# Optimization experiments

Measured on AMD Instinct MI355X. Metric: run time of the kernel, lower is better.

Reference implementation:

```python
import jax, jax.numpy as jnp
import numpy as np

B, D_W, D_C, D_P = 4096, 2048, 1024, 2048
RANK = D_W // 4  # 512, per A_U/A_V shapes (d_w, d_w//4)


def setup_inputs() -> dict:
    key = jax.random.key(0)
    ks = jax.random.split(key, 10)
    return {
        "w_prev": jax.random.normal(ks[0], (B, D_W), jnp.float32),
        "z_t": jax.random.normal(ks[1], (B, D_P), jnp.float32),
        "c_t": jax.random.normal(ks[2], (B, D_C), jnp.float32),
        # params (mirroring flax init: A_diag zeros, A_U/A_V normal(0.01),
        # Dense kernels lecun_normal-ish scale, zero biases)
        "A_diag": jnp.zeros((D_W,), jnp.float32),
        "A_U": 0.01 * jax.random.normal(ks[3], (D_W, RANK), jnp.float32),
        "A_V": 0.01 * jax.random.normal(ks[4], (D_W, RANK), jnp.float32),
        "W_mod": jax.random.normal(ks[5], (D_C, D_W), jnp.float32) / np.sqrt(D_C),
        "b_mod": jnp.zeros((D_W,), jnp.float32),
        "W_B": jax.random.normal(ks[6], (D_C + D_P, D_W), jnp.float32) / np.sqrt(D_C + D_P),
        "b_B": jnp.zeros((D_W,), jnp.float32),
    }


def reference(w_prev, z_t, c_t, A_diag, A_U, A_V, W_mod, b_mod, W_B, b_B):
    # A = diag(tanh(A_diag)*0.9) + A_U @ A_V^T, row-scaled by modulation.
    # Equivalent (same math) without materializing [B, d_w, d_w]:
    #   (A * m[:, :, None]) @ w = m * (a_diag * w + A_U @ (A_V^T @ w))
    a_diag = jnp.tanh(A_diag) * 0.9                              # [d_w]
    modulation = jnp.tanh(c_t @ W_mod + b_mod)                   # [B, d_w]
    Aw = a_diag * w_prev + (w_prev @ A_V) @ A_U.T                # [B, d_w]
    Bt = jnp.concatenate([c_t, z_t], axis=-1) @ W_B + b_B        # [B, d_w]
    return modulation * Aw + Bt
```

## Files before the change

### kernel.cpp

```cpp
#include <hip/hip_runtime.h>


#define DEV __device__ __forceinline__

typedef __bf16 v8bf __attribute__((ext_vector_type(8)));
typedef __bf16 v4bf __attribute__((ext_vector_type(4)));
typedef float  v4f  __attribute__((ext_vector_type(4)));

typedef __attribute__((address_space(1))) const unsigned int* as1_cuint_ptr;
typedef __attribute__((address_space(3))) unsigned int*       as3_uint_ptr;

DEV void async16(const void* g, void* l) {
  __builtin_amdgcn_global_load_lds(
      (as1_cuint_ptr)(unsigned long long)g,
      (as3_uint_ptr)(unsigned long long)l,
      16, 0, 0);
}

DEV float tanh_fast(float x) {
  x = fminf(15.f, fmaxf(-15.f, x));
  float e = __expf(2.f * x);
  return (e - 1.f) / (e + 1.f);
}

__global__ __launch_bounds__(256, 2) void prep_gemm(
    const float* __restrict__ w, const float* __restrict__ z,
    const float* __restrict__ c, const float* __restrict__ au,
    const float* __restrict__ av, const float* __restrict__ Wmod,
    const float* __restrict__ WB, const float* __restrict__ A_diag,
    __bf16* __restrict__ wb, __bf16* __restrict__ zb, __bf16* __restrict__ cb,
    __bf16* __restrict__ Wmodt, __bf16* __restrict__ WBt,
    __bf16* __restrict__ Mt) {
  __shared__ __align__(16) char smem[16384];
  int b = blockIdx.x;

  if (b < 256) {
    __bf16* As = (__bf16*)smem;
    __bf16* Bs = (__bf16*)(smem + 8192);
    const int tid = threadIdx.x, lane = tid & 63, wid = tid >> 6;
    const int wm = wid >> 1, wn = wid & 1, l16 = lane & 15, quad = lane >> 4;
    const int m0 = (b >> 4) * 128, n0 = (b & 15) * 128;
    const int qs = quad ^ ((l16 >> 1) & 3);
    const int row = tid >> 1, sp = (tid & 1) * 2;

    v4f acc[4][4];
#pragma unroll
    for (int i = 0; i < 4; ++i)
#pragma unroll
      for (int j = 0; j < 4; ++j) { v4f zz = {0, 0, 0, 0}; acc[i][j] = zz; }

    for (int k0 = 0; k0 < 512; k0 += 32) {
      __syncthreads();
#pragma unroll
      for (int ss = 0; ss < 2; ++ss) {
        const int s = sp + ss;
        const int gk = (s ^ ((row >> 1) & 3)) * 8;
        const float* pa = au + (size_t)(m0 + row) * 512 + k0 + gk;
        const float* pb = av + (size_t)(n0 + row) * 512 + k0 + gk;
        float4 a0 = *reinterpret_cast<const float4*>(pa);
        float4 a1 = *reinterpret_cast<const float4*>(pa + 4);
        float4 b0 = *reinterpret_cast<const float4*>(pb);
        float4 b1 = *reinterpret_cast<const float4*>(pb + 4);
        v8bf va, vb;
        va[0] = (__bf16)a0.x; va[1] = (__bf16)a0.y;
        va[2] = (__bf16)a0.z; va[3] = (__bf16)a0.w;
        va[4] = (__bf16)a1.x; va[5] = (__bf16)a1.y;
        va[6] = (__bf16)a1.z; va[7] = (__bf16)a1.w;
        vb[0] = (__bf16)b0.x; vb[1] = (__bf16)b0.y;
        vb[2] = (__bf16)b0.z; vb[3] = (__bf16)b0.w;
        vb[4] = (__bf16)b1.x; vb[5] = (__bf16)b1.y;
        vb[6] = (__bf16)b1.z; vb[7] = (__bf16)b1.w;
        *reinterpret_cast<v8bf*>(&As[row * 32 + s * 8]) = va;
        *reinterpret_cast<v8bf*>(&Bs[row * 32 + s * 8]) = vb;
      }
      __syncthreads();
      const v8bf* Ap = reinterpret_cast<const v8bf*>(As);
      const v8bf* Bp = reinterpret_cast<const v8bf*>(Bs);
      v8bf a[4], bb[4];
#pragma unroll
      for (int i = 0; i < 4; ++i) a[i] = Ap[(wm * 64 + i * 16 + l16) * 4 + qs];
#pragma unroll
      for (int j = 0; j < 4; ++j) bb[j] = Bp[(wn * 64 + j * 16 + l16) * 4 + qs];
#pragma unroll
      for (int i = 0; i < 4; ++i)
#pragma unroll
        for (int j = 0; j < 4; ++j)
          acc[i][j] = __builtin_amdgcn_mfma_f32_16x16x32_bf16(a[i], bb[j],
                                                              acc[i][j], 0, 0, 0);
    }

    const int mBase = m0 + wm * 64 + quad * 4;
    const int nBase = n0 + wn * 64 + l16;
#pragma unroll
    for (int j = 0; j < 4; ++j) {
      const int n = nBase + j * 16;
#pragma unroll
      for (int i = 0; i < 4; ++i)
#pragma unroll
        for (int r = 0; r < 4; ++r) {
          const int m = mBase + i * 16 + r;
          float v = acc[i][j][r];
          if (m == n) v += tanh_fast(A_diag[m]) * 0.9f;
          Mt[(size_t)m * 2048 + n] = (__bf16)v;
        }
    }
    return;
  }

  b -= 256;
  if (b < 20480) {
    const float* src; __bf16* dst; int off;
    if (b < 8192)       { src = w; dst = wb; off = b; }
    else if (b < 16384) { src = z; dst = zb; off = b - 8192; }
    else                { src = c; dst = cb; off = b - 16384; }
    size_t i = (size_t)off * 1024 + (size_t)threadIdx.x * 4;
    float4 v = *reinterpret_cast<const float4*>(src + i);
    v4bf o;
    o.x = (__bf16)v.x; o.y = (__bf16)v.y; o.z = (__bf16)v.z; o.w = (__bf16)v.w;
    *reinterpret_cast<v4bf*>(dst + i) = o;
    return;
  }

  b -= 20480;
  float (*t)[33] = (float(*)[33])smem;
  const float* src; __bf16* dst; int R;
  if (b < 2048) { src = Wmod; dst = Wmodt; R = 1024; }
  else          { b -= 2048; src = WB; dst = WBt; R = 3072; }
  const int c0 = (b & 63) * 32, r0 = (b >> 6) * 32;
  const int C = 2048;
  const int tx = threadIdx.x & 31, ty = threadIdx.x >> 5;
#pragma unroll
  for (int rr = 0; rr < 32; rr += 8)
    t[ty + rr][tx] = src[(size_t)(r0 + ty + rr) * C + c0 + tx];
  __syncthreads();
  const int orow = threadIdx.x >> 3;
  const int oc   = (threadIdx.x & 7) * 4;
  v4bf o;
  o.x = (__bf16)t[oc + 0][orow];
  o.y = (__bf16)t[oc + 1][orow];
  o.z = (__bf16)t[oc + 2][orow];
  o.w = (__bf16)t[oc + 3][orow];
  *reinterpret_cast<v4bf*>(&dst[(size_t)(c0 + orow) * R + r0 + oc]) = o;
}

__global__ __launch_bounds__(256, 2) void fused_main(
    const __bf16* __restrict__ c, const __bf16* __restrict__ z,
    const __bf16* __restrict__ w, const __bf16* __restrict__ Wmodt,
    const __bf16* __restrict__ Mt, const __bf16* __restrict__ WBt,
    const float* __restrict__ b_mod, const float* __restrict__ b_B,
    float* __restrict__ out) {
  constexpr int DC = 1024, DW = 2048, KB = 3072;
  __shared__ __align__(16) __bf16 As[128 * 128];
  __shared__ __align__(16) __bf16 Bs[128 * 128];

  const int tid = threadIdx.x, lane = tid & 63, wid = tid >> 6;
  const int wm = wid >> 1, wn = wid & 1, l16 = lane & 15, quad = lane >> 4;
  const int m0 = blockIdx.y * 128;
  const int n0 = blockIdx.x * 128;
  const int r4  = lane >> 4;
  const int s16 = lane & 15;

  v4f acc[4][4];
#pragma unroll
  for (int i = 0; i < 4; ++i)
#pragma unroll
    for (int j = 0; j < 4; ++j) { v4f zz = {0,0,0,0}; acc[i][j] = zz; }

  auto kstep = [&](const __bf16* gA, size_t lda, const __bf16* gB, size_t ldb,
                   int kA, int kB) {
    __syncthreads();
#pragma unroll
    for (int t = 0; t < 8; ++t) {
      const int row = wid * 32 + t * 4 + r4;
      const int gk = (s16 ^ (row & 15)) * 8;
      async16((const void*)(gA + (size_t)(m0 + row) * lda + kA + gk),
              (void*)&As[row * 128 + s16 * 8]);
      async16((const void*)(gB + (size_t)(n0 + row) * ldb + kB + gk),
              (void*)&Bs[row * 128 + s16 * 8]);
    }
    __syncthreads();
    const v8bf* Ap = reinterpret_cast<const v8bf*>(As);
    const v8bf* Bp = reinterpret_cast<const v8bf*>(Bs);
#pragma unroll
    for (int s = 0; s < 4; ++s) {
      const int rs = (s * 4 + quad) ^ l16;
      v8bf a[4], b[4];
#pragma unroll
      for (int i = 0; i < 4; ++i)
        a[i] = Ap[(wm * 64 + i * 16 + l16) * 16 + rs];
#pragma unroll
      for (int j = 0; j < 4; ++j)
        b[j] = Bp[(wn * 64 + j * 16 + l16) * 16 + rs];
#pragma unroll
      for (int i = 0; i < 4; ++i)
#pragma unroll
        for (int j = 0; j < 4; ++j)
          acc[i][j] = __builtin_amdgcn_mfma_f32_16x16x32_bf16(
              a[i], b[j], acc[i][j], 0, 0, 0);
    }
  };

  const int nBase = n0 + wn * 64 + l16;

  for (int k0 = 0; k0 < DC; k0 += 128) kstep(c, DC, Wmodt, DC, k0, k0);

  v4f mod_s[4][4];
#pragma unroll
  for (int j = 0; j < 4; ++j) {
    const float bn = b_mod[nBase + j * 16];
#pragma unroll
    for (int i = 0; i < 4; ++i) {
#pragma unroll
      for (int r = 0; r < 4; ++r)
        mod_s[i][j][r] = tanh_fast(acc[i][j][r] + bn);
      v4f zz = {0,0,0,0};
      acc[i][j] = zz;
    }
  }

  for (int k0 = 0; k0 < DW; k0 += 128) kstep(w, DW, Mt, DW, k0, k0);

#pragma unroll
  for (int i = 0; i < 4; ++i)
#pragma unroll
    for (int j = 0; j < 4; ++j) acc[i][j] *= mod_s[i][j];

  for (int k0 = 0; k0 < DC; k0 += 128) kstep(c, DC, WBt, KB, k0, k0);
  for (int k0 = DC; k0 < KB; k0 += 128) kstep(z, DW, WBt, KB, k0 - DC, k0);

  const int mBase = m0 + wm * 64 + quad * 4;
#pragma unroll
  for (int j = 0; j < 4; ++j) {
    const int n = nBase + j * 16;
    const float bn = b_B[n];
#pragma unroll
    for (int i = 0; i < 4; ++i)
#pragma unroll
      for (int r = 0; r < 4; ++r) {
        const int m = mBase + i * 16 + r;
        out[(size_t)m * DW + n] = acc[i][j][r] + bn;
      }
  }
}


extern "C" void kernel_launch(void* const* d_in, const int* in_sizes, int n_in,
                              void* d_out, int out_size, void* d_ws,
                              size_t ws_size, hipStream_t stream) {
  const float* w_prev = (const float*)d_in[0];
  const float* z_t    = (const float*)d_in[1];
  const float* c_t    = (const float*)d_in[2];
  const float* A_diag = (const float*)d_in[3];
  const float* A_U    = (const float*)d_in[4];
  const float* A_V    = (const float*)d_in[5];
  const float* W_mod  = (const float*)d_in[6];
  const float* b_mod  = (const float*)d_in[7];
  const float* W_B    = (const float*)d_in[8];
  const float* b_B    = (const float*)d_in[9];

  constexpr int Bsz = 4096, DW = 2048;
  const size_t MB = 1ull << 20;
  char* ws = (char*)d_ws;
  __bf16* w_bf  = (__bf16*)(ws + 0);
  __bf16* z_bf  = (__bf16*)(ws + 16 * MB);
  __bf16* c_bf  = (__bf16*)(ws + 32 * MB);
  __bf16* Wmodt = (__bf16*)(ws + 40 * MB);
  __bf16* WBt   = (__bf16*)(ws + 44 * MB);
  __bf16* Mt    = (__bf16*)(ws + 56 * MB);

  prep_gemm<<<28928, 256, 0, stream>>>(w_prev, z_t, c_t, A_U, A_V, W_mod, W_B,
                                       A_diag, w_bf, z_bf, c_bf, Wmodt, WBt,
                                       Mt);

  fused_main<<<dim3(DW / 128, Bsz / 128), 256, 0, stream>>>(
      c_bf, z_bf, w_bf, Wmodt, Mt, WBt, b_mod, b_B, (float*)d_out);
}
```

Measured before the change: 285.3 us.

## Pipeline main GEMM with triple-buffered async loads and 256x128 tiles

Rewrites the fused GEMM kernel to use 512-thread blocks with 256x128 output tiles, a 64-wide K step and a three-stage LDS ring, so async global-to-LDS loads for tile t+2 overlap the MFMA work on tile t. It also swizzles block order for L2 locality, keeps the modulation factor in bf16 registers, and makes the prep kernel grid-stride over fewer blocks. The aim is to hide the load-wait-compute serialization and per-step barriers of the old single-buffer loop. In exchange it needs more LDS and registers per block and uses hand-placed vmcnt waits and barriers, which could cost occupancy or break if the wait counts are wrong.

```diff
diff --git a/kernel.cpp b/kernel.cpp
--- a/kernel.cpp
+++ b/kernel.cpp
@@ -108,138 +108,206 @@
   }
 
   b -= 256;
-  if (b < 20480) {
-    const float* src; __bf16* dst; int off;
-    if (b < 8192)       { src = w; dst = wb; off = b; }
-    else if (b < 16384) { src = z; dst = zb; off = b - 8192; }
-    else                { src = c; dst = cb; off = b - 16384; }
-    size_t i = (size_t)off * 1024 + (size_t)threadIdx.x * 4;
-    float4 v = *reinterpret_cast<const float4*>(src + i);
-    v4bf o;
-    o.x = (__bf16)v.x; o.y = (__bf16)v.y; o.z = (__bf16)v.z; o.w = (__bf16)v.w;
-    *reinterpret_cast<v4bf*>(dst + i) = o;
+  if (b < 2048) {
+    for (int u = b; u < 20480; u += 2048) {
+      const float* src; __bf16* dst; int off;
+      if (u < 8192)       { src = w; dst = wb; off = u; }
+      else if (u < 16384) { src = z; dst = zb; off = u - 8192; }
+      else                { src = c; dst = cb; off = u - 16384; }
+      size_t i = (size_t)off * 1024 + (size_t)threadIdx.x * 4;
+      float4 v = *reinterpret_cast<const float4*>(src + i);
+      v4bf o;
+      o.x = (__bf16)v.x; o.y = (__bf16)v.y;
+      o.z = (__bf16)v.z; o.w = (__bf16)v.w;
+      *reinterpret_cast<v4bf*>(dst + i) = o;
+    }
     return;
   }
 
-  b -= 20480;
+  b -= 2048;
   float (*t)[33] = (float(*)[33])smem;
-  const float* src; __bf16* dst; int R;
-  if (b < 2048) { src = Wmod; dst = Wmodt; R = 1024; }
-  else          { b -= 2048; src = WB; dst = WBt; R = 3072; }
-  const int c0 = (b & 63) * 32, r0 = (b >> 6) * 32;
-  const int C = 2048;
   const int tx = threadIdx.x & 31, ty = threadIdx.x >> 5;
-#pragma unroll
-  for (int rr = 0; rr < 32; rr += 8)
-    t[ty + rr][tx] = src[(size_t)(r0 + ty + rr) * C + c0 + tx];
-  __syncthreads();
   const int orow = threadIdx.x >> 3;
   const int oc   = (threadIdx.x & 7) * 4;
-  v4bf o;
-  o.x = (__bf16)t[oc + 0][orow];
-  o.y = (__bf16)t[oc + 1][orow];
-  o.z = (__bf16)t[oc + 2][orow];
-  o.w = (__bf16)t[oc + 3][orow];
-  *reinterpret_cast<v4bf*>(&dst[(size_t)(c0 + orow) * R + r0 + oc]) = o;
-}
-
-__global__ __launch_bounds__(256, 2) void fused_main(
+  for (int u = b; u < 8192; u += 1024) {
+    const float* src; __bf16* dst; int R, uu = u;
+    if (uu < 2048) { src = Wmod; dst = Wmodt; R = 1024; }
+    else           { uu -= 2048; src = WB; dst = WBt; R = 3072; }
+    const int c0 = (uu & 63) * 32, r0 = (uu >> 6) * 32;
+    const int C = 2048;
+    __syncthreads();
+#pragma unroll
+    for (int rr = 0; rr < 32; rr += 8)
+      t[ty + rr][tx] = src[(size_t)(r0 + ty + rr) * C + c0 + tx];
+    __syncthreads();
+    v4bf o;
+    o.x = (__bf16)t[oc + 0][orow];
+    o.y = (__bf16)t[oc + 1][orow];
+    o.z = (__bf16)t[oc + 2][orow];
+    o.w = (__bf16)t[oc + 3][orow];
+    *reinterpret_cast<v4bf*>(&dst[(size_t)(c0 + orow) * R + r0 + oc]) = o;
+  }
+}
+
+__global__ __launch_bounds__(512, 2) void fused_main(
     const __bf16* __restrict__ c, const __bf16* __restrict__ z,
     const __bf16* __restrict__ w, const __bf16* __restrict__ Wmodt,
     const __bf16* __restrict__ Mt, const __bf16* __restrict__ WBt,
     const float* __restrict__ b_mod, const float* __restrict__ b_B,
     float* __restrict__ out) {
-  constexpr int DC = 1024, DW = 2048, KB = 3072;
-  __shared__ __align__(16) __bf16 As[128 * 128];
-  __shared__ __align__(16) __bf16 Bs[128 * 128];
+  constexpr int DC = 1024, DW = 2048, KB3 = 3072;
+  constexpr int ATE = 256 * 64;
+  constexpr int BTE = 128 * 64;
+  constexpr int NT = 96;
+  __shared__ __align__(16) __bf16 As[3 * ATE];
+  __shared__ __align__(16) __bf16 Bs[3 * BTE];
 
   const int tid = threadIdx.x, lane = tid & 63, wid = tid >> 6;
-  const int wm = wid >> 1, wn = wid & 1, l16 = lane & 15, quad = lane >> 4;
-  const int m0 = blockIdx.y * 128;
-  const int n0 = blockIdx.x * 128;
-  const int r4  = lane >> 4;
-  const int s16 = lane & 15;
+  const int wm = wid >> 1, wn = wid & 1;
+  const int l16 = lane & 15, quad = lane >> 4, l8 = l16 & 7;
+  const int s8 = tid & 7, rowi = tid >> 3;
+  const int gks = ((s8 ^ (rowi & 7)) << 3);
+
+  const int flat = blockIdx.y * 16 + blockIdx.x;
+  const int swz = (flat & 7) * 32 + (flat >> 3);
+  const int m0 = (swz >> 4) * 256;
+  const int n0 = (swz & 15) * 128;
+
+  const int nBase = n0 + wn * 64 + l16;
+  float bmodr[4], bBr[4];
+#pragma unroll
+  for (int j = 0; j < 4; ++j) {
+    bmodr[j] = b_mod[nBase + j * 16];
+    bBr[j]   = b_B[nBase + j * 16];
+  }
+
+  auto resolve = [&](int T, const __bf16*& gA, int& lda, int& kA,
+                     const __bf16*& gB, int& ldb, int& kB) {
+    if (T < 16)      { gA = c; lda = DC; kA = T << 6;        gB = Wmodt; ldb = DC;  kB = T << 6; }
+    else if (T < 48) { gA = w; lda = DW; kA = (T - 16) << 6; gB = Mt;    ldb = DW;  kB = (T - 16) << 6; }
+    else if (T < 64) { gA = c; lda = DC; kA = (T - 48) << 6; gB = WBt;   ldb = KB3; kB = (T - 48) << 6; }
+    else             { gA = z; lda = DW; kA = (T - 64) << 6; gB = WBt;   ldb = KB3; kB = DC + ((T - 64) << 6); }
+  };
+
+  auto stageA = [&](int T, int q0, int qn) {
+    const __bf16* gA; const __bf16* gB; int lda, ldb, kA, kB;
+    resolve(T, gA, lda, kA, gB, ldb, kB);
+    __bf16* Ab = &As[(T % 3) * ATE];
+#pragma unroll
+    for (int q = 0; q < 4; ++q) {
+      if (q < q0 || q >= q0 + qn) continue;
+      const int row = q * 64 + rowi;
+      async16((const void*)(gA + (size_t)(m0 + row) * lda + kA + gks),
+              (void*)&Ab[row * 64 + s8 * 8]);
+    }
+  };
+  auto stageB = [&](int T) {
+    const __bf16* gA; const __bf16* gB; int lda, ldb, kA, kB;
+    resolve(T, gA, lda, kA, gB, ldb, kB);
+    __bf16* Bb = &Bs[(T % 3) * BTE];
+#pragma unroll
+    for (int q = 0; q < 2; ++q) {
+      const int row = q * 64 + rowi;
+      async16((const void*)(gB + (size_t)(n0 + row) * ldb + kB + gks),
+              (void*)&Bb[row * 64 + s8 * 8]);
+    }
+  };
 
   v4f acc[4][4];
 #pragma unroll
   for (int i = 0; i < 4; ++i)
 #pragma unroll
-    for (int j = 0; j < 4; ++j) { v4f zz = {0,0,0,0}; acc[i][j] = zz; }
-
-  auto kstep = [&](const __bf16* gA, size_t lda, const __bf16* gB, size_t ldb,
-                   int kA, int kB) {
-    __syncthreads();
-#pragma unroll
-    for (int t = 0; t < 8; ++t) {
-      const int row = wid * 32 + t * 4 + r4;
-      const int gk = (s16 ^ (row & 15)) * 8;
-      async16((const void*)(gA + (size_t)(m0 + row) * lda + kA + gk),
-              (void*)&As[row * 128 + s16 * 8]);
-      async16((const void*)(gB + (size_t)(n0 + row) * ldb + kB + gk),
-              (void*)&Bs[row * 128 + s16 * 8]);
-    }
-    __syncthreads();
-    const v8bf* Ap = reinterpret_cast<const v8bf*>(As);
-    const v8bf* Bp = reinterpret_cast<const v8bf*>(Bs);
-#pragma unroll
-    for (int s = 0; s < 4; ++s) {
-      const int rs = (s * 4 + quad) ^ l16;
-      v8bf a[4], b[4];
+    for (int j = 0; j < 4; ++j) { v4f zz = {0, 0, 0, 0}; acc[i][j] = zz; }
+  v4bf mod_b[4][4];
+
+  stageA(0, 0, 4); stageB(0);
+  stageA(1, 0, 4); stageB(1);
+  asm volatile("s_waitcnt vmcnt(6)" ::: "memory");
+  __builtin_amdgcn_s_barrier();
+  asm volatile("" ::: "memory");
+
+  for (int t = 0; t < NT; ++t) {
+    const v8bf* Ap = reinterpret_cast<const v8bf*>(&As[(t % 3) * ATE]);
+    const v8bf* Bp = reinterpret_cast<const v8bf*>(&Bs[(t % 3) * BTE]);
+    const bool pre = (t + 2 < NT);
+
+    v8bf a0[4], b0[4];
+#pragma unroll
+    for (int i = 0; i < 4; ++i)
+      a0[i] = Ap[(wm * 64 + i * 16 + l16) * 8 + (quad ^ l8)];
+#pragma unroll
+    for (int j = 0; j < 4; ++j)
+      b0[j] = Bp[(wn * 64 + j * 16 + l16) * 8 + (quad ^ l8)];
+    if (pre) stageA(t + 2, 0, 3);
+    asm volatile("" ::: "memory");
+    __builtin_amdgcn_s_barrier();
+    __builtin_amdgcn_s_setprio(1);
+#pragma unroll
+    for (int i = 0; i < 4; ++i)
+#pragma unroll
+      for (int j = 0; j < 4; ++j)
+        acc[i][j] = __builtin_amdgcn_mfma_f32_16x16x32_bf16(a0[i], b0[j],
+                                                            acc[i][j], 0, 0, 0);
+    __builtin_amdgcn_s_setprio(0);
+    asm volatile("" ::: "memory");
+    __builtin_amdgcn_s_barrier();
+
+    v8bf a1[4], b1[4];
+#pragma unroll
+    for (int i = 0; i < 4; ++i)
+      a1[i] = Ap[(wm * 64 + i * 16 + l16) * 8 + ((4 + quad) ^ l8)];
+#pragma unroll
+    for (int j = 0; j < 4; ++j)
+      b1[j] = Bp[(wn * 64 + j * 16 + l16) * 8 + ((4 + quad) ^ l8)];
+    if (pre) { stageA(t + 2, 3, 1); stageB(t + 2); }
+    asm volatile("" ::: "memory");
+    __builtin_amdgcn_s_barrier();
+    __builtin_amdgcn_s_setprio(1);
+#pragma unroll
+    for (int i = 0; i < 4; ++i)
+#pragma unroll
+      for (int j = 0; j < 4; ++j)
+        acc[i][j] = __builtin_amdgcn_mfma_f32_16x16x32_bf16(a1[i], b1[j],
+                                                            acc[i][j], 0, 0, 0);
+    __builtin_amdgcn_s_setprio(0);
+    if (pre) asm volatile("s_waitcnt vmcnt(6)" ::: "memory");
+    else     asm volatile("s_waitcnt vmcnt(0)" ::: "memory");
+    __builtin_amdgcn_s_barrier();
+    asm volatile("" ::: "memory");
+
+    if (t == 15) {
 #pragma unroll
       for (int i = 0; i < 4; ++i)
-        a[i] = Ap[(wm * 64 + i * 16 + l16) * 16 + rs];
-#pragma unroll
-      for (int j = 0; j < 4; ++j)
-        b[j] = Bp[(wn * 64 + j * 16 + l16) * 16 + rs];
+#pragma unroll
+        for (int j = 0; j < 4; ++j) {
+          v4bf mb;
+#pragma unroll
+          for (int r = 0; r < 4; ++r)
+            mb[r] = (__bf16)tanh_fast(acc[i][j][r] + bmodr[j]);
+          mod_b[i][j] = mb;
+          v4f zz = {0, 0, 0, 0};
+          acc[i][j] = zz;
+        }
+    } else if (t == 47) {
 #pragma unroll
       for (int i = 0; i < 4; ++i)
 #pragma unroll
         for (int j = 0; j < 4; ++j)
-          acc[i][j] = __builtin_amdgcn_mfma_f32_16x16x32_bf16(
-              a[i], b[j], acc[i][j], 0, 0, 0);
-    }
-  };
-
-  const int nBase = n0 + wn * 64 + l16;
-
-  for (int k0 = 0; k0 < DC; k0 += 128) kstep(c, DC, Wmodt, DC, k0, k0);
-
-  v4f mod_s[4][4];
-#pragma unroll
-  for (int j = 0; j < 4; ++j) {
-    const float bn = b_mod[nBase + j * 16];
-#pragma unroll
-    for (int i = 0; i < 4; ++i) {
-#pragma unroll
-      for (int r = 0; r < 4; ++r)
-        mod_s[i][j][r] = tanh_fast(acc[i][j][r] + bn);
-      v4f zz = {0,0,0,0};
-      acc[i][j] = zz;
-    }
-  }
-
-  for (int k0 = 0; k0 < DW; k0 += 128) kstep(w, DW, Mt, DW, k0, k0);
-
-#pragma unroll
-  for (int i = 0; i < 4; ++i)
-#pragma unroll
-    for (int j = 0; j < 4; ++j) acc[i][j] *= mod_s[i][j];
-
-  for (int k0 = 0; k0 < DC; k0 += 128) kstep(c, DC, WBt, KB, k0, k0);
-  for (int k0 = DC; k0 < KB; k0 += 128) kstep(z, DW, WBt, KB, k0 - DC, k0);
+#pragma unroll
+          for (int r = 0; r < 4; ++r)
+            acc[i][j][r] *= (float)mod_b[i][j][r];
+    }
+  }
 
   const int mBase = m0 + wm * 64 + quad * 4;
 #pragma unroll
   for (int j = 0; j < 4; ++j) {
     const int n = nBase + j * 16;
-    const float bn = b_B[n];
-#pragma unroll
-    for (int i = 0; i < 4; ++i)
-#pragma unroll
-      for (int r = 0; r < 4; ++r) {
-        const int m = mBase + i * 16 + r;
-        out[(size_t)m * DW + n] = acc[i][j][r] + bn;
-      }
+#pragma unroll
+    for (int i = 0; i < 4; ++i)
+#pragma unroll
+      for (int r = 0; r < 4; ++r)
+        out[(size_t)(mBase + i * 16 + r) * DW + n] = acc[i][j][r] + bBr[j];
   }
 }
 
@@ -258,7 +326,6 @@
   const float* W_B    = (const float*)d_in[8];
   const float* b_B    = (const float*)d_in[9];
 
-  constexpr int Bsz = 4096, DW = 2048;
   const size_t MB = 1ull << 20;
   char* ws = (char*)d_ws;
   __bf16* w_bf  = (__bf16*)(ws + 0);
@@ -268,10 +335,10 @@
   __bf16* WBt   = (__bf16*)(ws + 44 * MB);
   __bf16* Mt    = (__bf16*)(ws + 56 * MB);
 
-  prep_gemm<<<28928, 256, 0, stream>>>(w_prev, z_t, c_t, A_U, A_V, W_mod, W_B,
-                                       A_diag, w_bf, z_bf, c_bf, Wmodt, WBt,
-                                       Mt);
-
-  fused_main<<<dim3(DW / 128, Bsz / 128), 256, 0, stream>>>(
+  prep_gemm<<<3328, 256, 0, stream>>>(w_prev, z_t, c_t, A_U, A_V, W_mod, W_B,
+                                      A_diag, w_bf, z_bf, c_bf, Wmodt, WBt,
+                                      Mt);
+
+  fused_main<<<dim3(16, 16), 512, 0, stream>>>(
       c_bf, z_bf, w_bf, Wmodt, Mt, WBt, b_mod, b_B, (float*)d_out);
 }
```

Result: slower. 323.4 us (+13.4%).
